# Optimization experiments

Measured on AMD Instinct MI355X. Metric: run time of the kernel, lower is better.

## Reference

```python
import jax, jax.numpy as jnp
import numpy as np

N = 4096
DEG = 16.0
KC = 64  # max closed-neighborhood size supported (deg~16 graph => safe)


def setup_inputs() -> dict:
    key = jax.random.key(0)
    ks = jax.random.split(key, 6)
    u = jax.random.uniform(ks[0], (N, N))
    upper = jnp.triu((u < (DEG / N)).astype(jnp.float32), k=1)
    adj = upper + upper.T  # symmetric 0/1, zero diagonal
    d = 64
    return {
        'adj': adj,
        'e_w': jax.random.normal(ks[1], (15, d), dtype=jnp.float32) * 0.25,
        'e_b': jnp.zeros((d,), jnp.float32),
        'w1': jax.random.normal(ks[2], (3, d, d), dtype=jnp.float32) * 0.125,
        'b1': jnp.zeros((3, d), jnp.float32),
        'w2': jax.random.normal(ks[3], (3, d, d), dtype=jnp.float32) * 0.125,
        'b2': jnp.zeros((3, d), jnp.float32),
        'eps': jnp.zeros((3,), jnp.float32),
    }


def cr_feat(adj):
    n = adj.shape[0]
    m = adj + jnp.eye(n, dtype=adj.dtype)  # closed-neighborhood indicator rows [N,N]
    k = m.sum(1)                            # |S_v|
    D = m @ adj                             # D[v,u] = degree of u inside S_v (A symmetric)
    E = 0.5 * jnp.sum(m * D, axis=1)        # edges inside S_v
    W = jnp.sum(m * D * (D - 1.0) * 0.5, axis=1)  # wedges inside S_v
    vals, idx = jax.lax.top_k(m, KC)        # members of S_v (padded)
    valid = (vals > 0.5).astype(adj.dtype)
    sub = adj[idx[:, :, None], idx[:, None, :]]        # [N,KC,KC] induced subgraph
    sub = sub * valid[:, :, None] * valid[:, None, :]
    T = jnp.einsum('vij,vjk,vki->v', sub, sub, sub) / 6.0  # triangles inside S_v
    f3 = T
    f2 = W - 3.0 * T
    f1 = E * (k - 2.0) - 2.0 * f2 - 3.0 * f3
    tot = k * (k - 1.0) * (k - 2.0) / 6.0   # C(k,3) = total triples
    f0 = tot - f1 - f2 - f3
    f = jnp.stack([f0, f1, f2, f3], axis=1)
    f = jnp.where((k >= 3.0)[:, None], f, 0.0)  # original skips |nb|<3
    return f / (jnp.sum(f, axis=1, keepdims=True) + 1e-10)


def ww_feat(adj):
    a2 = adj @ adj
    a4 = a2 @ a2                             # matrix_power(adj, 4)
    vals, _ = jax.lax.top_k(a4, 8)           # per-row sort desc, top 8
    return vals


def degree_feat(adj):
    d = adj.sum(1)
    diag_a2 = jnp.einsum('vu,uv->v', adj, adj)  # diag(A@A)
    return jnp.stack([d, d ** 2, diag_a2], axis=1)


def _forward(adj, e_w, e_b, w1, b1, w2, b2, eps):
    feats = jnp.concatenate([cr_feat(adj), ww_feat(adj), degree_feat(adj)], axis=1)  # [N,15]
    x = feats @ e_w + e_b
    for i in range(3):
        h = (1.0 + eps[i]) * x + adj @ x
        x = jax.nn.relu(h @ w1[i] + b1[i]) @ w2[i] + b2[i]
    return x.sum(0)


def reference(adj, e_w, e_b, w1, b1, w2, b2, eps):
    return _forward(adj, e_w, e_b, w1, b1, w2, b2, eps)
```

## Files before the change

### kernel.cpp

```cpp
#include <hip/hip_runtime.h>
#include <hip/hip_bf16.h>
#include <stdint.h>

#define NN 4096


__device__ __forceinline__ unsigned int wave_umax_bcast(unsigned int v) {
    int x = (int)v;
    x = max(x, __builtin_amdgcn_update_dpp(0, x, 0x111, 0xF, 0xF, true));
    x = max(x, __builtin_amdgcn_update_dpp(0, x, 0x112, 0xF, 0xF, true));
    x = max(x, __builtin_amdgcn_update_dpp(0, x, 0x114, 0xF, 0xF, true));
    x = max(x, __builtin_amdgcn_update_dpp(0, x, 0x118, 0xF, 0xF, true));
    x = max(x, __builtin_amdgcn_update_dpp(0, x, 0x142, 0xF, 0xF, true));
    x = max(x, __builtin_amdgcn_update_dpp(0, x, 0x143, 0xF, 0xF, true));
    return (unsigned int)__builtin_amdgcn_readlane(x, 63);
}

__global__ __launch_bounds__(256) void scan_k(const float* __restrict__ adj,
                                              int* __restrict__ nbr,
                                              int* __restrict__ deg,
                                              unsigned long long* __restrict__ abits,
                                              float* __restrict__ feats) {
    __shared__ int nlist[4][64];
    int tid = threadIdx.x;
    int wv = tid >> 6, ln = tid & 63;
    int v = blockIdx.x * 4 + wv;
    size_t rb = (size_t)v * NN;
    int total = 0;
    unsigned long long w0 = 0;
    const float4* row4 = (const float4*)(adj + rb);
    for (int base = 0; base < NN; base += 256) {
        float4 f = row4[(base >> 2) + ln];
        int q4 = (base >> 8) << 2;
        #pragma unroll
        for (int j = 0; j < 4; j++) {
            float vj = (j == 0) ? f.x : (j == 1) ? f.y : (j == 2) ? f.z : f.w;
            unsigned long long m = __ballot(vj > 0.5f);
            if (vj > 0.5f) {
                int pos = total + __popcll(m & ((1ull << ln) - 1ull));
                if (pos < 64) nlist[wv][pos] = base + 4 * ln + j;
            }
            if (ln == q4 + j) w0 = m;
            total += __popcll(m);
        }
    }
    abits[(size_t)v * 64 + ln] = w0;
    int degL = min(total, 64);
    if (ln < degL) nbr[v * 64 + ln] = nlist[wv][ln];
    if (ln == 0) {
        deg[v] = total;
        float degf = (float)total;
        feats[v * 16 + 12] = degf;
        feats[v * 16 + 13] = degf * degf;
        feats[v * 16 + 14] = degf;
    }
}

__global__ __launch_bounds__(256) void cra2_k(const unsigned long long* __restrict__ abits,
                                              const int* __restrict__ nbr,
                                              const int* __restrict__ deg,
                                              unsigned int* __restrict__ a3n,
                                              unsigned int* __restrict__ side,
                                              unsigned int* __restrict__ scnt,
                                              float* __restrict__ feats) {
    __shared__ __align__(64) unsigned int smem[NN + 132 + 648];
    int tid = threadIdx.x;
    int bid = blockIdx.x;
    int wv = tid >> 6, ln = tid & 63;

    if (bid < NN) {
        unsigned int* acc   = smem;
        int* us             = (int*)(smem + NN);
        int* dus            = (int*)(smem + NN + 64);
        unsigned int* wsumS = smem + NN + 128;
        unsigned int* srcL  = smem + NN + 132;
        int v = bid;
        uint4 z = {0u, 0u, 0u, 0u};
        #pragma unroll
        for (int i = 0; i < 4; i++) ((uint4*)acc)[tid + 256 * i] = z;
        int dv = min(deg[v], 64);
        if (tid < dv) {
            int u = nbr[v * 64 + tid];
            us[tid] = u;
            dus[tid] = min(deg[u], 64);
        }
        __syncthreads();
        for (int p = tid; p < dv * 64; p += 256) {
            int i = p >> 6, wi = p & 63;
            if (wi < dus[i]) atomicAdd(&acc[nbr[us[i] * 64 + wi]], 1u);
        }
        __syncthreads();
        unsigned int myw[16];
        int local = 0;
        #pragma unroll
        for (int m = 0; m < 16; m++) {
            unsigned int a = acc[tid + 256 * m];
            myw[m] = a;
            local += (a != 0u);
        }
        int incl = local;
        #pragma unroll
        for (int off = 1; off < 64; off <<= 1) {
            int n = __shfl_up(incl, off, 64);
            if (ln >= off) incl += n;
        }
        if (ln == 63) wsumS[wv] = (unsigned int)incl;
        __syncthreads();
        unsigned int wpre = 0, nsrc = 0;
        #pragma unroll
        for (int q = 0; q < 4; q++) {
            unsigned int s = wsumS[q];
            if (q < wv) wpre += s;
            nsrc += s;
        }
        unsigned int pos = wpre + (unsigned int)(incl - local);
        #pragma unroll
        for (int m = 0; m < 16; m++) {
            unsigned int a = myw[m];
            if (a) {
                unsigned int col = (unsigned int)tid + 256u * m;
                unsigned int dgu = (unsigned int)min(deg[col], 64);
                if (pos < 640u) srcL[pos] = (a << 19) | (dgu << 12) | col;
                pos++;
            }
        }
        if (nsrc > 640u) nsrc = 640u;
        __syncthreads();
        #pragma unroll
        for (int i = 0; i < 4; i++) ((uint4*)acc)[tid + 256 * i] = z;
        int nsrc8 = (((int)nsrc + 7) >> 3) << 3;
        if (tid < nsrc8 - (int)nsrc) srcL[(int)nsrc + tid] = 0u;
        __syncthreads();
        for (int i0 = wv * 8; i0 < nsrc8; i0 += 32) {
            uint4 qa = *(const uint4*)&srcL[i0];
            uint4 qb = *(const uint4*)&srcL[i0 + 4];
            int c1 = (int)((qa.x >> 12) & 0x7Fu);
            int c2 = c1 + (int)((qa.y >> 12) & 0x7Fu);
            int c3 = c2 + (int)((qa.z >> 12) & 0x7Fu);
            int c4 = c3 + (int)((qa.w >> 12) & 0x7Fu);
            int c5 = c4 + (int)((qb.x >> 12) & 0x7Fu);
            int c6 = c5 + (int)((qb.y >> 12) & 0x7Fu);
            int c7 = c6 + (int)((qb.z >> 12) & 0x7Fu);
            int tot = c7 + (int)((qb.w >> 12) & 0x7Fu);
            unsigned int s0 = ((qa.x & 0xFFFu) * 64u)                                | (qa.x & 0xFFF80000u);
            unsigned int s1 = ((((qa.y & 0xFFFu) * 64u) - (unsigned int)c1) & 0x7FFFFu) | (qa.y & 0xFFF80000u);
            unsigned int s2 = ((((qa.z & 0xFFFu) * 64u) - (unsigned int)c2) & 0x7FFFFu) | (qa.z & 0xFFF80000u);
            unsigned int s3 = ((((qa.w & 0xFFFu) * 64u) - (unsigned int)c3) & 0x7FFFFu) | (qa.w & 0xFFF80000u);
            unsigned int s4 = ((((qb.x & 0xFFFu) * 64u) - (unsigned int)c4) & 0x7FFFFu) | (qb.x & 0xFFF80000u);
            unsigned int s5 = ((((qb.y & 0xFFFu) * 64u) - (unsigned int)c5) & 0x7FFFFu) | (qb.y & 0xFFF80000u);
            unsigned int s6 = ((((qb.z & 0xFFFu) * 64u) - (unsigned int)c6) & 0x7FFFFu) | (qb.z & 0xFFF80000u);
            unsigned int s7 = ((((qb.w & 0xFFFu) * 64u) - (unsigned int)c7) & 0x7FFFFu) | (qb.w & 0xFFF80000u);
            for (int g = ln; g < tot; g += 64) {
                unsigned int sel = (g < c1) ? s0 : (g < c2) ? s1 : (g < c3) ? s2 : (g < c4) ? s3
                                 : (g < c5) ? s4 : (g < c6) ? s5 : (g < c7) ? s6 : s7;
                unsigned int idx = (sel + (unsigned int)g) & 0x7FFFFu;
                atomicAdd(&acc[nbr[idx]], sel >> 19);
            }
        }
        __syncthreads();
        unsigned int wAn = 0, wBn = 0, ovm = 0;
        #pragma unroll
        for (int i2 = 0; i2 < 8; i2++) {
            unsigned int a = acc[16 * tid + i2];
            wAn |= min(a, 15u) << (4 * i2);
            ovm |= (a > 15u ? 1u : 0u) << i2;
        }
        #pragma unroll
        for (int i2 = 0; i2 < 8; i2++) {
            unsigned int a = acc[16 * tid + 8 + i2];
            wBn |= min(a, 15u) << (4 * i2);
            ovm |= (a > 15u ? 1u : 0u) << (8 + i2);
        }
        {
            uint2 nw; nw.x = wAn; nw.y = wBn;
            ((uint2*)(a3n + (size_t)v * 512))[tid] = nw;
        }
        int lov = __popc(ovm);
        int inc2 = lov;
        #pragma unroll
        for (int off = 1; off < 64; off <<= 1) {
            int n = __shfl_up(inc2, off, 64);
            if (ln >= off) inc2 += n;
        }
        if (ln == 63) wsumS[wv] = (unsigned int)inc2;
        __syncthreads();
        unsigned int wpre2 = 0, totS = 0;
        #pragma unroll
        for (int q = 0; q < 4; q++) {
            unsigned int s = wsumS[q];
            if (q < wv) wpre2 += s;
            totS += s;
        }
        unsigned int pos2 = wpre2 + (unsigned int)(inc2 - lov);
        unsigned int* sideR = side + (size_t)v * 192;
        while (ovm) {
            int i2 = __ffs(ovm) - 1;
            ovm &= ovm - 1;
            unsigned int col = (unsigned int)(16 * tid + i2);
            unsigned int a = acc[col];
            if (pos2 < 192u) sideR[pos2] = ((a - 15u) << 16) | col;
            pos2++;
        }
        if (tid == 0) scnt[v] = min(totS, 192u);
    } else {
        unsigned long long* rows = (unsigned long long*)smem;
        int* mems = (int*)(smem + 1024);
        int v = (bid - NN) * 4 + wv;

        int dv = deg[v];
        int degL = min(dv, 64);
        int c = min(dv + 1, 64);

        int nl = (ln < degL) ? nbr[v * 64 + ln] : 0;
        int isless = (ln < degL && nl < v) ? 1 : 0;
        int pos = isless;
        #pragma unroll
        for (int off = 32; off; off >>= 1) pos += __shfl_xor(pos, off, 64);

        int mem = 0;
        if (ln < c) {
            if (ln < pos)       mem = nl;
            else if (ln == pos) mem = v;
            else                mem = nbr[v * 64 + ln - 1];
        }
        mems[wv * 64 + ln] = mem;
        __syncthreads();

        unsigned long long mask = 0ull;
        {
            const unsigned long long* rowb = abits + (size_t)mem * 64;
            for (int j = 0; j < c; j++) {
                int mj = mems[wv * 64 + j];
                unsigned long long w = rowb[((mj >> 8) << 2) | (mj & 3)];
                mask |= ((w >> ((mj >> 2) & 63)) & 1ull) << j;
            }
        }
        if (ln >= c) mask = 0ull;
        rows[wv * 64 + ln] = mask;
        __syncthreads();

        int tpart = 0;
        float epart = 0.f, wpart = 0.f;
        if (ln < c) {
            unsigned long long mm = mask;
            while (mm) {
                int j = __ffsll(mm) - 1;
                mm &= mm - 1;
                tpart += __popcll(mask & rows[wv * 64 + j]);
            }
            if (ln != pos) {
                int cn = __popcll(rows[wv * 64 + pos] & mask);
                float D2 = (float)cn + 1.0f;
                epart = D2;
                wpart = D2 * (D2 - 1.0f) * 0.5f;
            }
        }
        float es = epart, wsum2 = wpart;
        int ts = tpart;
        #pragma unroll
        for (int off = 32; off; off >>= 1) {
            es += __shfl_xor(es, off, 64);
            wsum2 += __shfl_xor(wsum2, off, 64);
            ts += __shfl_xor(ts, off, 64);
        }

        if (ln == 0) {
            float degf = (float)dv;
            float k = degf + 1.0f;
            float E = 0.5f * (es + degf);
            float W = wsum2 + degf * (degf - 1.0f) * 0.5f;
            float T = (float)ts / 6.0f;
            float f3 = T;
            float f2 = W - 3.0f * T;
            float f1 = E * (k - 2.0f) - 2.0f * f2 - 3.0f * f3;
            float tot2 = k * (k - 1.0f) * (k - 2.0f) / 6.0f;
            float f0 = tot2 - f1 - f2 - f3;
            if (k < 3.0f) { f0 = f1 = f2 = f3 = 0.f; }
            float s = f0 + f1 + f2 + f3 + 1e-10f;
            feats[v * 16 + 0] = f0 / s;
            feats[v * 16 + 1] = f1 / s;
            feats[v * 16 + 2] = f2 / s;
            feats[v * 16 + 3] = f3 / s;
        }
    }
}

__global__ __launch_bounds__(512) void a4row_k(const unsigned int* __restrict__ a3n,
                                               const unsigned int* __restrict__ side,
                                               const unsigned int* __restrict__ scnt,
                                               const int* __restrict__ deg,
                                               const int* __restrict__ nbr,
                                               const float* __restrict__ feats,
                                               const float* __restrict__ e_w,
                                               const float* __restrict__ e_b,
                                               float* __restrict__ x0) {
    __shared__ unsigned int sacc[NN];
    __shared__ unsigned int sbase[64];
    __shared__ unsigned int sbs[64];
    __shared__ unsigned int sS[64];
    __shared__ unsigned int wtops[64];
    int tid = threadIdx.x;
    int wv = tid >> 6, ln = tid & 63;
    int v = blockIdx.x;

    {
        uint4 z = {0u, 0u, 0u, 0u};
        ((uint4*)sacc)[tid] = z;
        ((uint4*)sacc)[tid + 512] = z;
    }
    int dvv = min(deg[v], 64);
    if (tid < dvv) {
        unsigned int u = (unsigned int)nbr[v * 64 + tid];
        sbase[tid] = u * 512u;
        sbs[tid]   = u * 192u;
        sS[tid]    = scnt[u];
    }
    __syncthreads();

    for (int i = wv; i < dvv; i += 8) {
        int ns = (int)sS[i];
        const unsigned int* sp = side + sbs[i];
        for (int g2 = ln; g2 < ns; g2 += 64) {
            unsigned int e = sp[g2];
            atomicAdd(&sacc[e & 0xFFFu], e >> 16);
        }
    }

    unsigned int aE = 0, aO = 0;
    unsigned int SE0 = 0, SE1 = 0, SO0 = 0, SO1 = 0;
    for (int s0 = 0; s0 < dvv; s0 += 16) {
        int se = min(s0 + 16, dvv);
        for (int s = s0; s < se; s++) {
            unsigned int w = a3n[sbase[s] + (unsigned int)tid];
            aE += w & 0x0F0F0F0Fu;
            aO += (w >> 4) & 0x0F0F0F0Fu;
        }
        SE0 += __builtin_amdgcn_perm(0u, aE, 0x0c010c00u);
        SE1 += __builtin_amdgcn_perm(0u, aE, 0x0c030c02u);
        SO0 += __builtin_amdgcn_perm(0u, aO, 0x0c010c00u);
        SO1 += __builtin_amdgcn_perm(0u, aO, 0x0c030c02u);
        aE = 0; aO = 0;
    }
    __syncthreads();

    uint4 s03 = ((uint4*)sacc)[2 * tid];
    uint4 s47 = ((uint4*)sacc)[2 * tid + 1];
    unsigned int vv[8];
    vv[0] = (SE0 & 0xFFFFu) + s03.x;
    vv[1] = (SO0 & 0xFFFFu) + s03.y;
    vv[2] = (SE0 >> 16)     + s03.z;
    vv[3] = (SO0 >> 16)     + s03.w;
    vv[4] = (SE1 & 0xFFFFu) + s47.x;
    vv[5] = (SO1 & 0xFFFFu) + s47.y;
    vv[6] = (SE1 >> 16)     + s47.z;
    vv[7] = (SO1 >> 16)     + s47.w;

    unsigned int best[8];
    #pragma unroll
    for (int q = 0; q < 8; q++) best[q] = 0u;
    #pragma unroll
    for (int m = 0; m < 8; m++) {
        unsigned int val = vv[m];
        if (val > best[7]) {
            best[7] = val;
            #pragma unroll
            for (int s = 7; s > 0; s--) {
                if (best[s] > best[s - 1]) {
                    unsigned int t2 = best[s - 1]; best[s - 1] = best[s]; best[s] = t2;
                } else break;
            }
        }
    }

    unsigned int wave_val = 0u;
    #pragma unroll
    for (int r = 0; r < 8; r++) {
        unsigned int m = wave_umax_bcast(best[0]);
        unsigned long long bb = __ballot(best[0] == m);
        int src = __ffsll(bb) - 1;
        if (ln == src) {
            #pragma unroll
            for (int s = 0; s < 7; s++) best[s] = best[s + 1];
            best[7] = 0u;
        }
        if (ln == r) wave_val = m;
    }
    if (ln < 8) wtops[wv * 8 + ln] = wave_val;
    __syncthreads();

    if (wv == 0) {
        unsigned int cand = wtops[ln];
        unsigned int myv = 0u;
        #pragma unroll
        for (int r = 0; r < 8; r++) {
            unsigned int m = wave_umax_bcast(cand);
            unsigned long long bb = __ballot(cand == m);
            int src = __ffsll(bb) - 1;
            if (ln == src) cand = 0u;
            if (ln == r) myv = m;
        }
        int d = ln;
        float s = e_b[d];
        s += feats[v * 16 + 0]  * e_w[0 * 64 + d];
        s += feats[v * 16 + 1]  * e_w[1 * 64 + d];
        s += feats[v * 16 + 2]  * e_w[2 * 64 + d];
        s += feats[v * 16 + 3]  * e_w[3 * 64 + d];
        #pragma unroll
        for (int j = 0; j < 8; j++) {
            float mj = (float)(unsigned int)__shfl((int)myv, j, 64);
            s += mj * e_w[(4 + j) * 64 + d];
        }
        s += feats[v * 16 + 12] * e_w[12 * 64 + d];
        s += feats[v * 16 + 13] * e_w[13 * 64 + d];
        s += feats[v * 16 + 14] * e_w[14 * 64 + d];
        x0[(size_t)v * 64 + d] = s;
    }
}

__global__ __launch_bounds__(256) void layer_k(const float* __restrict__ xin,
                                               float* __restrict__ xout,
                                               const float* __restrict__ w1,
                                               const float* __restrict__ b1,
                                               const float* __restrict__ w2,
                                               const float* __restrict__ b2,
                                               const float* __restrict__ eps,
                                               const int* __restrict__ nbr,
                                               const int* __restrict__ deg,
                                               float* __restrict__ out,
                                               int li) {
    __shared__ float wL[4096];
    __shared__ float h[4][64], t[4][64];
    int tid = threadIdx.x;
    int wv = tid >> 6, d = tid & 63;
    int v = blockIdx.x * 4 + wv;

    {
        const float4* src = (const float4*)(w1 + li * 4096);
        #pragma unroll
        for (int i = 0; i < 4; i++) ((float4*)wL)[tid + 256 * i] = src[tid + 256 * i];
    }

    float xv = xin[(size_t)v * 64 + d];
    int dv = min(deg[v], 64);
    const int* nl = nbr + v * 64;
    float agg = 0.f;
    int j = 0;
    for (; j + 4 <= dv; j += 4) {
        int n0 = nl[j], n1 = nl[j + 1], n2 = nl[j + 2], n3 = nl[j + 3];
        float a0 = xin[(size_t)n0 * 64 + d];
        float a1 = xin[(size_t)n1 * 64 + d];
        float a2v = xin[(size_t)n2 * 64 + d];
        float a3 = xin[(size_t)n3 * 64 + d];
        agg += (a0 + a1) + (a2v + a3);
    }
    for (; j < dv; j++) agg += xin[(size_t)nl[j] * 64 + d];
    float hv = (1.0f + eps[li]) * xv + agg;
    h[wv][d] = hv;
    __syncthreads();

    float s = b1[li * 64 + d];
    #pragma unroll 8
    for (int k = 0; k < 64; k++) s += h[wv][k] * wL[k * 64 + d];
    s = fmaxf(s, 0.f);
    t[wv][d] = s;
    __syncthreads();

    {
        const float4* src = (const float4*)(w2 + li * 4096);
        #pragma unroll
        for (int i = 0; i < 4; i++) ((float4*)wL)[tid + 256 * i] = src[tid + 256 * i];
    }
    __syncthreads();

    float o = b2[li * 64 + d];
    #pragma unroll 8
    for (int k = 0; k < 64; k++) o += t[wv][k] * wL[k * 64 + d];
    if (li == 2) {
        h[wv][d] = o;
        __syncthreads();
        if (wv == 0)
            atomicAdd(&out[d], (h[0][d] + h[1][d]) + (h[2][d] + h[3][d]));
    } else {
        xout[(size_t)v * 64 + d] = o;
    }
}

extern "C" void kernel_launch(void* const* d_in, const int* in_sizes, int n_in,
                              void* d_out, int out_size, void* d_ws, size_t ws_size,
                              hipStream_t stream) {
    const float* adj = (const float*)d_in[0];
    const float* e_w = (const float*)d_in[1];
    const float* e_b = (const float*)d_in[2];
    const float* w1  = (const float*)d_in[3];
    const float* b1  = (const float*)d_in[4];
    const float* w2  = (const float*)d_in[5];
    const float* b2  = (const float*)d_in[6];
    const float* eps = (const float*)d_in[7];
    float* out = (float*)d_out;

    char* ws = (char*)d_ws;
    unsigned int*       a3n     = (unsigned int*)(ws);
    unsigned int*       side    = (unsigned int*)(ws + 8388608);
    unsigned int*       scnt    = (unsigned int*)(ws + 11534336);
    int*                nbr     = (int*)(ws + 25165824);
    int*                deg     = (int*)(ws + 26214400);
    float*              feats   = (float*)(ws + 26247168);
    float*              x0      = (float*)(ws + 26509312);
    float*              x1      = (float*)(ws + 27557888);
    unsigned long long* abits   = (unsigned long long*)(ws + 28868608);

    hipMemsetAsync(out, 0, 64 * sizeof(float), stream);
    scan_k<<<1024, 256, 0, stream>>>(adj, nbr, deg, abits, feats);
    cra2_k<<<5120, 256, 0, stream>>>(abits, nbr, deg, a3n, side, scnt, feats);
    a4row_k<<<4096, 512, 0, stream>>>(a3n, side, scnt, deg, nbr, feats, e_w, e_b, x0);
    layer_k<<<1024, 256, 0, stream>>>(x0, x1, w1, b1, w2, b2, eps, nbr, deg, out, 0);
    layer_k<<<1024, 256, 0, stream>>>(x1, x0, w1, b1, w2, b2, eps, nbr, deg, out, 1);
    layer_k<<<1024, 256, 0, stream>>>(x0, x1, w1, b1, w2, b2, eps, nbr, deg, out, 2);
}
```

Before: 255.7 us.

## Swizzle LDS accumulator indices and keep layer weights in registers

The scan kernel's shared-memory accumulator is now indexed through an XOR swizzle, which spreads the strided reads (16*tid+i) and scattered atomics across LDS banks to cut bank conflicts. The layer kernel drops its 16KB shared weight tile: each lane loads its own weight column into 64 registers, reads h/t as float4 broadcasts, and prefetches w2 before the barrier. This frees LDS and removes a barrier so more blocks can be resident, at the cost of higher register pressure and uncoalesced strided global weight loads.

```diff
diff --git a/kernel.cpp b/kernel.cpp
--- a/kernel.cpp
+++ b/kernel.cpp
@@ -4,6 +4,8 @@
 
 #define NN 4096
 
+
+#define SW(x) ((unsigned int)(x) ^ ((((unsigned int)(x)) >> 5) & 31u))
 
 __device__ __forceinline__ unsigned int wave_umax_bcast(unsigned int v) {
     int x = (int)v;
@@ -87,14 +89,14 @@
         __syncthreads();
         for (int p = tid; p < dv * 64; p += 256) {
             int i = p >> 6, wi = p & 63;
-            if (wi < dus[i]) atomicAdd(&acc[nbr[us[i] * 64 + wi]], 1u);
+            if (wi < dus[i]) atomicAdd(&acc[SW(nbr[us[i] * 64 + wi])], 1u);
         }
         __syncthreads();
         unsigned int myw[16];
         int local = 0;
         #pragma unroll
         for (int m = 0; m < 16; m++) {
-            unsigned int a = acc[tid + 256 * m];
+            unsigned int a = acc[SW(tid + 256 * m)];
             myw[m] = a;
             local += (a != 0u);
         }
@@ -154,20 +156,20 @@
                 unsigned int sel = (g < c1) ? s0 : (g < c2) ? s1 : (g < c3) ? s2 : (g < c4) ? s3
                                  : (g < c5) ? s4 : (g < c6) ? s5 : (g < c7) ? s6 : s7;
                 unsigned int idx = (sel + (unsigned int)g) & 0x7FFFFu;
-                atomicAdd(&acc[nbr[idx]], sel >> 19);
+                atomicAdd(&acc[SW(nbr[idx])], sel >> 19);
             }
         }
         __syncthreads();
         unsigned int wAn = 0, wBn = 0, ovm = 0;
         #pragma unroll
         for (int i2 = 0; i2 < 8; i2++) {
-            unsigned int a = acc[16 * tid + i2];
+            unsigned int a = acc[SW(16 * tid + i2)];
             wAn |= min(a, 15u) << (4 * i2);
             ovm |= (a > 15u ? 1u : 0u) << i2;
         }
         #pragma unroll
         for (int i2 = 0; i2 < 8; i2++) {
-            unsigned int a = acc[16 * tid + 8 + i2];
+            unsigned int a = acc[SW(16 * tid + 8 + i2)];
             wBn |= min(a, 15u) << (4 * i2);
             ovm |= (a > 15u ? 1u : 0u) << (8 + i2);
         }
@@ -197,7 +199,7 @@
             int i2 = __ffs(ovm) - 1;
             ovm &= ovm - 1;
             unsigned int col = (unsigned int)(16 * tid + i2);
-            unsigned int a = acc[col];
+            unsigned int a = acc[SW(col)];
             if (pos2 < 192u) sideR[pos2] = ((a - 15u) << 16) | col;
             pos2++;
         }
@@ -417,27 +419,27 @@
     }
 }
 
-__global__ __launch_bounds__(256) void layer_k(const float* __restrict__ xin,
-                                               float* __restrict__ xout,
-                                               const float* __restrict__ w1,
-                                               const float* __restrict__ b1,
-                                               const float* __restrict__ w2,
-                                               const float* __restrict__ b2,
-                                               const float* __restrict__ eps,
-                                               const int* __restrict__ nbr,
-                                               const int* __restrict__ deg,
-                                               float* __restrict__ out,
-                                               int li) {
-    __shared__ float wL[4096];
-    __shared__ float h[4][64], t[4][64];
+__global__ __launch_bounds__(256, 4) void layer_k(const float* __restrict__ xin,
+                                                  float* __restrict__ xout,
+                                                  const float* __restrict__ w1,
+                                                  const float* __restrict__ b1,
+                                                  const float* __restrict__ w2,
+                                                  const float* __restrict__ b2,
+                                                  const float* __restrict__ eps,
+                                                  const int* __restrict__ nbr,
+                                                  const int* __restrict__ deg,
+                                                  float* __restrict__ out,
+                                                  int li) {
+    __shared__ __align__(16) float h[4][64], t[4][64];
     int tid = threadIdx.x;
     int wv = tid >> 6, d = tid & 63;
     int v = blockIdx.x * 4 + wv;
 
+    float wr[64];
     {
-        const float4* src = (const float4*)(w1 + li * 4096);
-        #pragma unroll
-        for (int i = 0; i < 4; i++) ((float4*)wL)[tid + 256 * i] = src[tid + 256 * i];
+        const float* w1c = w1 + li * 4096 + d;
+        #pragma unroll
+        for (int k = 0; k < 64; k++) wr[k] = w1c[k * 64];
     }
 
     float xv = xin[(size_t)v * 64 + d];
@@ -459,22 +461,33 @@
     __syncthreads();
 
     float s = b1[li * 64 + d];
-    #pragma unroll 8
-    for (int k = 0; k < 64; k++) s += h[wv][k] * wL[k * 64 + d];
+    #pragma unroll
+    for (int k4 = 0; k4 < 16; k4++) {
+        float4 hq = *(const float4*)&h[wv][k4 * 4];
+        s += hq.x * wr[k4 * 4 + 0];
+        s += hq.y * wr[k4 * 4 + 1];
+        s += hq.z * wr[k4 * 4 + 2];
+        s += hq.w * wr[k4 * 4 + 3];
+    }
     s = fmaxf(s, 0.f);
     t[wv][d] = s;
+
+    {
+        const float* w2c = w2 + li * 4096 + d;
+        #pragma unroll
+        for (int k = 0; k < 64; k++) wr[k] = w2c[k * 64];
+    }
     __syncthreads();
 
-    {
-        const float4* src = (const float4*)(w2 + li * 4096);
-        #pragma unroll
-        for (int i = 0; i < 4; i++) ((float4*)wL)[tid + 256 * i] = src[tid + 256 * i];
-    }
-    __syncthreads();
-
     float o = b2[li * 64 + d];
-    #pragma unroll 8
-    for (int k = 0; k < 64; k++) o += t[wv][k] * wL[k * 64 + d];
+    #pragma unroll
+    for (int k4 = 0; k4 < 16; k4++) {
+        float4 tq = *(const float4*)&t[wv][k4 * 4];
+        o += tq.x * wr[k4 * 4 + 0];
+        o += tq.y * wr[k4 * 4 + 1];
+        o += tq.z * wr[k4 * 4 + 2];
+        o += tq.w * wr[k4 * 4 + 3];
+    }
     if (li == 2) {
         h[wv][d] = o;
         __syncthreads();
```

Result: no change. 259.4 us (+1.4%).

## Simplify A^3 scatter to pair-per-64-thread mapping and interleave nibble-packed layout

Applied to the files above, without the earlier changes.

Replaces the prefix-sum based 8-source batched scatter loop with a simpler mapping in which each 64-thread slot handles two source vertices, 32 lanes each, and one lane serially covers neighbors beyond 32. It also changes the nibble-packed a3n layout so each thread packs columns strided by 512 rather than 16 contiguous columns. Shared-memory reads then become conflict-free and global stores coalesced, and the consumer kernel's sacc reads are updated to match. The aim is less index-selection overhead and fewer LDS bank conflicts, but high-degree sources now do serial tail work.

```diff
diff --git a/kernel.cpp b/kernel.cpp
--- a/kernel.cpp
+++ b/kernel.cpp
@@ -63,7 +63,7 @@
                                               unsigned int* __restrict__ side,
                                               unsigned int* __restrict__ scnt,
                                               float* __restrict__ feats) {
-    __shared__ __align__(64) unsigned int smem[NN + 132 + 648];
+    __shared__ __align__(64) unsigned int smem[NN + 132 + 640];
     int tid = threadIdx.x;
     int bid = blockIdx.x;
     int wv = tid >> 6, ln = tid & 63;
@@ -128,53 +128,38 @@
         __syncthreads();
         #pragma unroll
         for (int i = 0; i < 4; i++) ((uint4*)acc)[tid + 256 * i] = z;
-        int nsrc8 = (((int)nsrc + 7) >> 3) << 3;
-        if (tid < nsrc8 - (int)nsrc) srcL[(int)nsrc + tid] = 0u;
-        __syncthreads();
-        for (int i0 = wv * 8; i0 < nsrc8; i0 += 32) {
-            uint4 qa = *(const uint4*)&srcL[i0];
-            uint4 qb = *(const uint4*)&srcL[i0 + 4];
-            int c1 = (int)((qa.x >> 12) & 0x7Fu);
-            int c2 = c1 + (int)((qa.y >> 12) & 0x7Fu);
-            int c3 = c2 + (int)((qa.z >> 12) & 0x7Fu);
-            int c4 = c3 + (int)((qa.w >> 12) & 0x7Fu);
-            int c5 = c4 + (int)((qb.x >> 12) & 0x7Fu);
-            int c6 = c5 + (int)((qb.y >> 12) & 0x7Fu);
-            int c7 = c6 + (int)((qb.z >> 12) & 0x7Fu);
-            int tot = c7 + (int)((qb.w >> 12) & 0x7Fu);
-            unsigned int s0 = ((qa.x & 0xFFFu) * 64u)                                | (qa.x & 0xFFF80000u);
-            unsigned int s1 = ((((qa.y & 0xFFFu) * 64u) - (unsigned int)c1) & 0x7FFFFu) | (qa.y & 0xFFF80000u);
-            unsigned int s2 = ((((qa.z & 0xFFFu) * 64u) - (unsigned int)c2) & 0x7FFFFu) | (qa.z & 0xFFF80000u);
-            unsigned int s3 = ((((qa.w & 0xFFFu) * 64u) - (unsigned int)c3) & 0x7FFFFu) | (qa.w & 0xFFF80000u);
-            unsigned int s4 = ((((qb.x & 0xFFFu) * 64u) - (unsigned int)c4) & 0x7FFFFu) | (qb.x & 0xFFF80000u);
-            unsigned int s5 = ((((qb.y & 0xFFFu) * 64u) - (unsigned int)c5) & 0x7FFFFu) | (qb.y & 0xFFF80000u);
-            unsigned int s6 = ((((qb.z & 0xFFFu) * 64u) - (unsigned int)c6) & 0x7FFFFu) | (qb.z & 0xFFF80000u);
-            unsigned int s7 = ((((qb.w & 0xFFFu) * 64u) - (unsigned int)c7) & 0x7FFFFu) | (qb.w & 0xFFF80000u);
-            for (int g = ln; g < tot; g += 64) {
-                unsigned int sel = (g < c1) ? s0 : (g < c2) ? s1 : (g < c3) ? s2 : (g < c4) ? s3
-                                 : (g < c5) ? s4 : (g < c6) ? s5 : (g < c7) ? s6 : s7;
-                unsigned int idx = (sel + (unsigned int)g) & 0x7FFFFu;
-                atomicAdd(&acc[nbr[idx]], sel >> 19);
-            }
-        }
-        __syncthreads();
-        unsigned int wAn = 0, wBn = 0, ovm = 0;
-        #pragma unroll
-        for (int i2 = 0; i2 < 8; i2++) {
-            unsigned int a = acc[16 * tid + i2];
-            wAn |= min(a, 15u) << (4 * i2);
-            ovm |= (a > 15u ? 1u : 0u) << i2;
-        }
-        #pragma unroll
-        for (int i2 = 0; i2 < 8; i2++) {
-            unsigned int a = acc[16 * tid + 8 + i2];
-            wBn |= min(a, 15u) << (4 * i2);
-            ovm |= (a > 15u ? 1u : 0u) << (8 + i2);
-        }
-        {
-            uint2 nw; nw.x = wAn; nw.y = wBn;
-            ((uint2*)(a3n + (size_t)v * 512))[tid] = nw;
-        }
+        __syncthreads();
+        int lim64 = (((int)nsrc + 1) >> 1) << 6;
+        for (int q = tid; q < lim64; q += 256) {
+            int s = ((q >> 6) << 1) | ((q >> 5) & 1);
+            int j = q & 31;
+            if (s < (int)nsrc) {
+                unsigned int e = srcL[s];
+                int dgu = (int)((e >> 12) & 0x7Fu);
+                unsigned int w = e >> 19;
+                const int* nru = nbr + (e & 0xFFFu) * 64;
+                if (j < dgu) atomicAdd(&acc[nru[j]], w);
+                if (j == 31) {
+                    for (int jj = 32; jj < dgu; jj++) atomicAdd(&acc[nru[jj]], w);
+                }
+            }
+        }
+        __syncthreads();
+        unsigned int wA = 0, wB = 0, ovm = 0;
+        #pragma unroll
+        for (int k = 0; k < 8; k++) {
+            unsigned int a = acc[tid + 512 * k];
+            wA |= min(a, 15u) << (4 * k);
+            ovm |= (a > 15u ? 1u : 0u) << k;
+        }
+        #pragma unroll
+        for (int k = 0; k < 8; k++) {
+            unsigned int a = acc[tid + 256 + 512 * k];
+            wB |= min(a, 15u) << (4 * k);
+            ovm |= (a > 15u ? 1u : 0u) << (8 + k);
+        }
+        a3n[(size_t)v * 512 + tid] = wA;
+        a3n[(size_t)v * 512 + tid + 256] = wB;
         int lov = __popc(ovm);
         int inc2 = lov;
         #pragma unroll
@@ -196,7 +181,8 @@
         while (ovm) {
             int i2 = __ffs(ovm) - 1;
             ovm &= ovm - 1;
-            unsigned int col = (unsigned int)(16 * tid + i2);
+            unsigned int col = (i2 < 8) ? (unsigned int)(tid + 512 * i2)
+                                        : (unsigned int)(tid + 256 + 512 * (i2 - 8));
             unsigned int a = acc[col];
             if (pos2 < 192u) sideR[pos2] = ((a - 15u) << 16) | col;
             pos2++;
@@ -343,17 +329,15 @@
     }
     __syncthreads();
 
-    uint4 s03 = ((uint4*)sacc)[2 * tid];
-    uint4 s47 = ((uint4*)sacc)[2 * tid + 1];
     unsigned int vv[8];
-    vv[0] = (SE0 & 0xFFFFu) + s03.x;
-    vv[1] = (SO0 & 0xFFFFu) + s03.y;
-    vv[2] = (SE0 >> 16)     + s03.z;
-    vv[3] = (SO0 >> 16)     + s03.w;
-    vv[4] = (SE1 & 0xFFFFu) + s47.x;
-    vv[5] = (SO1 & 0xFFFFu) + s47.y;
-    vv[6] = (SE1 >> 16)     + s47.z;
-    vv[7] = (SO1 >> 16)     + s47.w;
+    vv[0] = (SE0 & 0xFFFFu) + sacc[tid];
+    vv[1] = (SO0 & 0xFFFFu) + sacc[tid + 512];
+    vv[2] = (SE0 >> 16)     + sacc[tid + 1024];
+    vv[3] = (SO0 >> 16)     + sacc[tid + 1536];
+    vv[4] = (SE1 & 0xFFFFu) + sacc[tid + 2048];
+    vv[5] = (SO1 & 0xFFFFu) + sacc[tid + 2560];
+    vv[6] = (SE1 >> 16)     + sacc[tid + 3072];
+    vv[7] = (SO1 >> 16)     + sacc[tid + 3584];
 
     unsigned int best[8];
     #pragma unroll
```

After: 253.2 us. About the same (-1.0%).
